# Performance work log

Hardware: AMD Instinct MI355X
Metric: run time of the kernel (lower is better)

The kernel has to match this reference:

```python
import jax, jax.numpy as jnp
import numpy as np

B, T, C = 4, 2048, 1024
H, HS = 16, 64  # n_heads, head_size; H*HS == C


def setup_inputs() -> dict:
    key = jax.random.key(0)
    ks = jax.random.split(key, 6)
    s = 0.02
    x = jax.random.normal(ks[0], (B, T, C), dtype=jnp.float32)
    Wq = jax.random.normal(ks[1], (H, C, HS), dtype=jnp.float32) * s
    Wk = jax.random.normal(ks[2], (H, C, HS), dtype=jnp.float32) * s
    Wv = jax.random.normal(ks[3], (H, C, HS), dtype=jnp.float32) * s
    Wo = jax.random.normal(ks[4], (C, C), dtype=jnp.float32) * s
    bo = jnp.zeros((C,), dtype=jnp.float32)
    return {"x": x, "Wq": Wq, "Wk": Wk, "Wv": Wv, "Wo": Wo, "bo": bo}


def reference(x, Wq, Wk, Wv, Wo, bo):
    # batched multi-head causal attention (math identical to per-head loop)
    q = jnp.einsum('btc,hcd->bhtd', x, Wq)  # [B,H,T,HS]
    k = jnp.einsum('btc,hcd->bhtd', x, Wk)
    v = jnp.einsum('btc,hcd->bhtd', x, Wv)
    scale = 1.0 / jnp.sqrt(jnp.asarray(HS, x.dtype))
    scores = jnp.einsum('bhtd,bhsd->bhts', q, k) * scale  # [B,H,T,T]
    causal = jnp.tril(jnp.ones((T, T), dtype=bool))
    scores = jnp.where(causal, scores, jnp.asarray(-jnp.inf, scores.dtype))
    attn = jax.nn.softmax(scores, axis=-1)
    out = jnp.einsum('bhts,bhsd->bhtd', attn, v)  # [B,H,T,HS]
    # concat heads along feature dim (head order == module list order)
    out = out.transpose(0, 2, 1, 3).reshape(B, T, C)
    return out @ Wo.T + bo
```

## Files before the change

### kernel.cpp

```cpp
#include <hip/hip_runtime.h>

typedef __attribute__((ext_vector_type(8))) short v8s;
typedef __attribute__((ext_vector_type(4))) short v4s;
typedef __attribute__((ext_vector_type(4))) float v4f;

static __device__ __forceinline__ short f2bf(float f) {
  union { float f; unsigned u; } c; c.f = f;
  unsigned r = c.u + 0x7fffu + ((c.u >> 16) & 1u);
  return (short)(r >> 16);
}

static __device__ __forceinline__ unsigned pk_bf16(float a, float b) {
  union { float f; unsigned u; } ca, cb; ca.f = a; cb.f = b;
  return ((ca.u + 0x8000u) >> 16) | ((cb.u + 0x8000u) & 0xffff0000u);
}

#if __has_builtin(__builtin_amdgcn_exp2f)
#define EXP2(x) __builtin_amdgcn_exp2f(x)
#else
#define EXP2(x) exp2f(x)
#endif

#define GLDS(gp, lp) __builtin_amdgcn_global_load_lds( \
    (const __attribute__((address_space(1))) void*)(gp), \
    (__attribute__((address_space(3))) void*)(lp), 16, 0, 0)


__global__ __launch_bounds__(256) void cast_f32_bf16(const float* __restrict__ src,
                                                     short* __restrict__ dst) {
  int idx = (blockIdx.x * 256 + threadIdx.x) * 4;
  float4 v = *(const float4*)(src + idx);
  v4s o; o.x = f2bf(v.x); o.y = f2bf(v.y); o.z = f2bf(v.z); o.w = f2bf(v.w);
  *(v4s*)(dst + idx) = o;
}

__global__ __launch_bounds__(256) void build_wt(const float* __restrict__ Wq,
                                                const float* __restrict__ Wk,
                                                const float* __restrict__ Wv,
                                                short* __restrict__ Wt) {
  __shared__ float tile[64][65];
  int blk = blockIdx.x;
  int sel = blk >> 8, rest = blk & 255;
  int h = rest >> 4, kt = rest & 15;
  const float* W = (sel == 0) ? Wq : ((sel == 1) ? Wk : Wv);
  int k0 = kt * 64;
  int tid = threadIdx.x;
  for (int i = 0; i < 4; ++i) {
    int c = i * 256 + tid;
    int row = c >> 4, c4 = (c & 15) * 4;
    float4 v = *(const float4*)(W + (size_t)h * 65536 + (size_t)(k0 + row) * 64 + c4);
    tile[row][c4 + 0] = v.x; tile[row][c4 + 1] = v.y;
    tile[row][c4 + 2] = v.z; tile[row][c4 + 3] = v.w;
  }
  __syncthreads();
  for (int i = 0; i < 2; ++i) {
    int c = i * 256 + tid;
    int d = c >> 3, k8 = (c & 7) * 8;
    v8s o;
    for (int j = 0; j < 8; ++j) o[j] = f2bf(tile[k8 + j][d]);
    *(v8s*)(Wt + (size_t)(sel * 1024 + h * 64 + d) * 1024 + k0 + k8) = o;
  }
}


__global__ __launch_bounds__(512) void gemm_qkv(const short* __restrict__ Xb,
                                                const short* __restrict__ Wt,
                                                short* __restrict__ Qo,
                                                short* __restrict__ Ko,
                                                short* __restrict__ Vt) {
  __shared__ short lds[49152];
  const int tid = threadIdx.x;
  const int lane = tid & 63, quad = lane >> 4, l16 = lane & 15;
  const int wave = tid >> 6;
  const int m0 = blockIdx.x * 256, n0 = blockIdx.y * 128;
  const int wm = (wave >> 1) * 64, wn = (wave & 1) * 64;

  const int r0 = tid >> 2, cbs = (tid & 3) ^ ((r0 >> 1) & 3);
  const size_t offA0 = (size_t)(m0 + r0) * 1024 + cbs * 8;
  const size_t offB0 = (size_t)(n0 + r0) * 1024 + cbs * 8;

  int aoff[4], boff[4];
#pragma unroll
  for (int mt = 0; mt < 4; ++mt) {
    int row = wm + mt * 16 + l16;
    aoff[mt] = row * 32 + (quad ^ ((row >> 1) & 3)) * 8;
  }
#pragma unroll
  for (int nt = 0; nt < 4; ++nt) {
    int row = wn + nt * 16 + l16;
    boff[nt] = row * 32 + (quad ^ ((row >> 1) & 3)) * 8;
  }

  v4f acc[4][4];
#pragma unroll
  for (int i = 0; i < 4; ++i)
#pragma unroll
    for (int j = 0; j < 4; ++j) acc[i][j] = (v4f){0.f, 0.f, 0.f, 0.f};

#pragma unroll
  for (int t = 0; t < 3; ++t) {
    GLDS(Xb + offA0 + t * 32, lds + t * 8192 + tid * 8);
    GLDS(Xb + offA0 + 131072 + t * 32, lds + t * 8192 + 4096 + tid * 8);
    GLDS(Wt + offB0 + t * 32, lds + 32768 + t * 4096 + tid * 8);
  }
  asm volatile("s_waitcnt vmcnt(6)" ::: "memory");
  __builtin_amdgcn_s_barrier();

#pragma unroll 4
  for (int t = 0; t < 32; ++t) {
    const int p = t & 3;
    int tn = t + 3; if (tn > 31) tn = 31;
    const int pn = (t + 3) & 3;
    const short* lAp = lds + p * 8192;
    const short* lBp = lds + 32768 + p * 4096;

    GLDS(Xb + offA0 + tn * 32, lds + pn * 8192 + tid * 8);
    GLDS(Xb + offA0 + 131072 + tn * 32, lds + pn * 8192 + 4096 + tid * 8);
    v8s a[4], b[2];
#pragma unroll
    for (int mt = 0; mt < 4; ++mt) a[mt] = *(const v8s*)(lAp + aoff[mt]);
    b[0] = *(const v8s*)(lBp + boff[0]);
    b[1] = *(const v8s*)(lBp + boff[1]);
    __builtin_amdgcn_s_setprio(1);
#pragma unroll
    for (int mt = 0; mt < 4; ++mt) {
      acc[mt][0] = __builtin_amdgcn_mfma_f32_16x16x32_bf16(a[mt], b[0], acc[mt][0], 0, 0, 0);
      acc[mt][1] = __builtin_amdgcn_mfma_f32_16x16x32_bf16(a[mt], b[1], acc[mt][1], 0, 0, 0);
    }
    __builtin_amdgcn_s_setprio(0);

    GLDS(Wt + offB0 + tn * 32, lds + 32768 + pn * 4096 + tid * 8);
    b[0] = *(const v8s*)(lBp + boff[2]);
    b[1] = *(const v8s*)(lBp + boff[3]);
    __builtin_amdgcn_s_setprio(1);
#pragma unroll
    for (int mt = 0; mt < 4; ++mt) {
      acc[mt][2] = __builtin_amdgcn_mfma_f32_16x16x32_bf16(a[mt], b[0], acc[mt][2], 0, 0, 0);
      acc[mt][3] = __builtin_amdgcn_mfma_f32_16x16x32_bf16(a[mt], b[1], acc[mt][3], 0, 0, 0);
    }
    __builtin_amdgcn_s_setprio(0);

    asm volatile("s_waitcnt vmcnt(6) lgkmcnt(0)" ::: "memory");
    __builtin_amdgcn_s_barrier();
  }

  const int selu = n0 >> 10;
  if (selu < 2) {
    short* obase = (selu == 0) ? Qo : Ko;
#pragma unroll
    for (int nt = 0; nt < 4; ++nt) {
      int n = (n0 + wn + nt * 16 + l16) & 1023;
      int h = n >> 6, d = n & 63;
#pragma unroll
      for (int mt = 0; mt < 4; ++mt) {
        int m = m0 + wm + mt * 16 + quad * 4;
        int b_ = m >> 11, tt = m & 2047;
        size_t base = (size_t)((b_ * 16 + h) * 2048 + tt) * 64 + d;
#pragma unroll
        for (int r = 0; r < 4; ++r)
          obase[base + (size_t)r * 64] = f2bf(acc[mt][nt][r]);
      }
    }
  } else {
#pragma unroll
    for (int nt = 0; nt < 4; ++nt) {
      int n = (n0 + wn + nt * 16 + l16) & 1023;
      int h = n >> 6, d = n & 63;
#pragma unroll
      for (int mt = 0; mt < 4; ++mt) {
        int m = m0 + wm + mt * 16 + quad * 4;
        int b_ = m >> 11, tt = m & 2047;
        int2 dw;
        dw.x = (int)pk_bf16(acc[mt][nt][0], acc[mt][nt][1]);
        dw.y = (int)pk_bf16(acc[mt][nt][2], acc[mt][nt][3]);
        *(int2*)(Vt + ((size_t)(b_ * 16 + h) * 64 + d) * 2048 + tt) = dw;
      }
    }
  }
}


__global__ __launch_bounds__(256, 2) void attn(const short* __restrict__ Q,
                                               const short* __restrict__ K,
                                               const short* __restrict__ Vt,
                                               short* __restrict__ AO) {
  __shared__ short lK[64 * 64];
  __shared__ short lV[64 * 64];
  __shared__ short lP[4 * 32 * 72];
  const int tid = threadIdx.x;
  const int w = tid >> 6, lane = tid & 63, quad = lane >> 4, l16 = lane & 15;
  const int bh = blockIdx.x & 63, pr = blockIdx.x >> 6;
  const float kexp = 0.18033688011112042f;
  const unsigned psel = 0x07060302u;
  short* pw = lP + w * (32 * 72);
  const size_t qkbase = (size_t)bh * 2048 * 64;
  const size_t vtbase = (size_t)bh * 64 * 2048;
  const int b_ = bh >> 4, h = bh & 15;

  const int r0 = tid >> 3, cp = tid & 7;
  const int cl0 = cp ^ (r0 & 7);
  const int r1 = r0 + 32;
  const int cl1 = cp ^ (r1 & 7);

  const int swz = l16 & 7;
  const int ph0 = (quad ^ swz) * 8;
  const int ph1 = ((quad + 4) ^ swz) * 8;

  for (int phase = 0; phase < 2; ++phase) {
    const int c = phase ? (15 - pr) : pr;
    const int qc = c * 128 + w * 32;

    v8s bQ[2][2];
#pragma unroll
    for (int qs = 0; qs < 2; ++qs) {
      const short* qb = Q + qkbase + (size_t)(qc + qs * 16 + l16) * 64 + quad * 8;
      bQ[qs][0] = *(const v8s*)(qb);
      bQ[qs][1] = *(const v8s*)(qb + 32);
    }
    v4f accO[2][4];
#pragma unroll
    for (int qs = 0; qs < 2; ++qs)
      for (int g = 0; g < 4; ++g) accO[qs][g] = (v4f){0.f, 0.f, 0.f, 0.f};
    float lrun[2] = {0.f, 0.f};

    const int nst = 2 * c + 2;
    for (int kt = 0; kt < nst; ++kt) {
      const int kb = kt * 64;
      __syncthreads();
      GLDS(K + qkbase + (size_t)(kb + r0) * 64 + cl0 * 8, lK + tid * 8);
      GLDS(K + qkbase + (size_t)(kb + r1) * 64 + cl1 * 8, lK + tid * 8 + 2048);
      GLDS(Vt + vtbase + (size_t)r0 * 2048 + kb + cl0 * 8, lV + tid * 8);
      GLDS(Vt + vtbase + (size_t)r1 * 2048 + kb + cl1 * 8, lV + tid * 8 + 2048);
      __syncthreads();

      const bool act0 = kb < qc + 16;
      const bool act1 = kb < qc + 32;
      if (!act1) continue;

      v8s aK[4][2];
#pragma unroll
      for (int mt = 0; mt < 4; ++mt) {
        const short* kr = lK + (mt * 16 + l16) * 64;
        aK[mt][0] = *(const v8s*)(kr + ph0);
        aK[mt][1] = *(const v8s*)(kr + ph1);
      }
#pragma unroll
      for (int qs = 0; qs < 2; ++qs) {
        if (qs == 0 ? !act0 : false) continue;
        const int rbase = qc + qs * 16;
        v4f sT[4];
#pragma unroll
        for (int mt = 0; mt < 4; ++mt) {
          v4f t = (v4f){0.f, 0.f, 0.f, 0.f};
          t = __builtin_amdgcn_mfma_f32_16x16x32_bf16(aK[mt][0], bQ[qs][0], t, 0, 0, 0);
          t = __builtin_amdgcn_mfma_f32_16x16x32_bf16(aK[mt][1], bQ[qs][1], t, 0, 0, 0);
          sT[mt] = t;
        }
        if (kb + 63 >= rbase) {
          const int kq = kb + quad * 4 - (rbase + l16);
#pragma unroll
          for (int mt = 0; mt < 4; ++mt)
#pragma unroll
            for (int r = 0; r < 4; ++r)
              if (kq + mt * 16 + r > 0) sT[mt][r] = -__builtin_inff();
        }
        float ls = lrun[qs];
#pragma unroll
        for (int mt = 0; mt < 4; ++mt) {
          float p0 = EXP2(sT[mt][0] * kexp);
          float p1 = EXP2(sT[mt][1] * kexp);
          float p2 = EXP2(sT[mt][2] * kexp);
          float p3 = EXP2(sT[mt][3] * kexp);
          ls += (p0 + p1) + (p2 + p3);
          int2 dw;
          dw.x = (int)__builtin_amdgcn_perm(__float_as_uint(p1), __float_as_uint(p0), psel);
          dw.y = (int)__builtin_amdgcn_perm(__float_as_uint(p3), __float_as_uint(p2), psel);
          *(int2*)&pw[(qs * 16 + l16) * 72 + mt * 16 + quad * 4] = dw;
        }
        lrun[qs] = ls;
      }
      v8s aV[4][2];
#pragma unroll
      for (int g = 0; g < 4; ++g) {
        const short* vr = lV + (g * 16 + l16) * 64;
        aV[g][0] = *(const v8s*)(vr + ph0);
        aV[g][1] = *(const v8s*)(vr + ph1);
      }
#pragma unroll
      for (int qs = 0; qs < 2; ++qs) {
        if (qs == 0 ? !act0 : false) continue;
        v8s bP0 = *(const v8s*)&pw[(qs * 16 + l16) * 72 + quad * 8];
        v8s bP1 = *(const v8s*)&pw[(qs * 16 + l16) * 72 + 32 + quad * 8];
#pragma unroll
        for (int g = 0; g < 4; ++g) {
          accO[qs][g] = __builtin_amdgcn_mfma_f32_16x16x32_bf16(aV[g][0], bP0, accO[qs][g], 0, 0, 0);
          accO[qs][g] = __builtin_amdgcn_mfma_f32_16x16x32_bf16(aV[g][1], bP1, accO[qs][g], 0, 0, 0);
        }
      }
    }

#pragma unroll
    for (int qs = 0; qs < 2; ++qs) {
      float ls = lrun[qs];
      ls += __shfl_xor(ls, 16);
      ls += __shfl_xor(ls, 32);
      float inv = __builtin_amdgcn_rcpf(ls);
      int t = qc + qs * 16 + l16;
      short* ao = AO + ((size_t)(b_ * 2048 + t)) * 1024 + h * 64 + quad * 4;
#pragma unroll
      for (int g = 0; g < 4; ++g) {
        int2 dw;
        dw.x = (int)pk_bf16(accO[qs][g][0] * inv, accO[qs][g][1] * inv);
        dw.y = (int)pk_bf16(accO[qs][g][2] * inv, accO[qs][g][3] * inv);
        *(int2*)(ao + g * 16) = dw;
      }
    }
  }
}


__global__ __launch_bounds__(256) void gemm_out(const short* __restrict__ AO,
                                                const short* __restrict__ Wot,
                                                const float* __restrict__ bo,
                                                float* __restrict__ out) {
  __shared__ short lA[128 * 32];
  __shared__ short lB[128 * 32];
  const int tid = threadIdx.x;
  const int lane = tid & 63, quad = lane >> 4, l16 = lane & 15;
  const int wave = tid >> 6;
  const int m0 = blockIdx.x * 128, n0 = blockIdx.y * 128;
  const int wm = (wave >> 1) * 64, wn = (wave & 1) * 64;
  v4f acc[4][4];
  for (int i = 0; i < 4; ++i)
    for (int j = 0; j < 4; ++j) acc[i][j] = (v4f){0.f, 0.f, 0.f, 0.f};

  for (int k0 = 0; k0 < 1024; k0 += 32) {
    __syncthreads();
    for (int i = 0; i < 2; ++i) {
      int c = i * 256 + tid;
      int row = c >> 2, kc = c & 3;
      GLDS(AO + (size_t)(m0 + row) * 1024 + k0 + kc * 8, lA + c * 8);
      GLDS(Wot + (size_t)(n0 + row) * 1024 + k0 + kc * 8, lB + c * 8);
    }
    __syncthreads();
    v8s a[4], b[4];
    for (int mt = 0; mt < 4; ++mt) a[mt] = *(const v8s*)&lA[(wm + mt * 16 + l16) * 32 + quad * 8];
    for (int nt = 0; nt < 4; ++nt) b[nt] = *(const v8s*)&lB[(wn + nt * 16 + l16) * 32 + quad * 8];
    for (int mt = 0; mt < 4; ++mt)
      for (int nt = 0; nt < 4; ++nt)
        acc[mt][nt] = __builtin_amdgcn_mfma_f32_16x16x32_bf16(a[mt], b[nt], acc[mt][nt], 0, 0, 0);
  }

  for (int nt = 0; nt < 4; ++nt) {
    int n = n0 + wn + nt * 16 + l16;
    float bias = bo[n];
    for (int mt = 0; mt < 4; ++mt)
      for (int r = 0; r < 4; ++r) {
        int m = m0 + wm + mt * 16 + quad * 4 + r;
        out[(size_t)m * 1024 + n] = acc[mt][nt][r] + bias;
      }
  }
}


extern "C" void kernel_launch(void* const* d_in, const int* in_sizes, int n_in,
                              void* d_out, int out_size, void* d_ws, size_t ws_size,
                              hipStream_t stream) {
  const float* x  = (const float*)d_in[0];
  const float* Wq = (const float*)d_in[1];
  const float* Wk = (const float*)d_in[2];
  const float* Wv = (const float*)d_in[3];
  const float* Wo = (const float*)d_in[4];
  const float* bo = (const float*)d_in[5];
  float* out = (float*)d_out;
  char* ws = (char*)d_ws;

  short* Xb  = (short*)(ws);
  short* Wt  = (short*)(ws + (16u << 20));
  short* Wot = (short*)(ws + (22u << 20));
  short* Q   = (short*)(ws + (24u << 20));
  short* K   = (short*)(ws + (40u << 20));
  short* Vt  = (short*)(ws + (56u << 20));

  cast_f32_bf16<<<8192, 256, 0, stream>>>(x, Xb);
  cast_f32_bf16<<<1024, 256, 0, stream>>>(Wo, Wot);
  build_wt<<<768, 256, 0, stream>>>(Wq, Wk, Wv, Wt);
  gemm_qkv<<<dim3(32, 24), 512, 0, stream>>>(Xb, Wt, Q, K, Vt);
  attn<<<dim3(512), 256, 0, stream>>>(Q, K, Vt, Xb);
  gemm_out<<<dim3(64, 8), 256, 0, stream>>>(Xb, Wot, bo, out);
}
```

Measured before the change: 243.0 us.

## Restructure QKV GEMM into 256x256 tiles with K=64 phased ping-pong pipeline

The fused QKV projection GEMM moves from 256x128 tiles with K=32 steps and a 4-stage ring to 256x256 tiles with K=64 steps. LDS is split into two ping-pong buffers, and each k-tile runs four phases that interleave half-tile global-to-LDS staging with MFMA blocks, with barriers and priority set around each phase. Each wave now holds an 8x4 accumulator block, which should roughly double arithmetic intensity per LDS load. The grid is 1D with a remap that groups tiles sharing the same activation rows. The larger register footprint and 128KB of LDS limit the kernel to one block per CU, and with 384 blocks the tail wave may be uneven.

```diff
diff --git a/kernel.cpp b/kernel.cpp
--- a/kernel.cpp
+++ b/kernel.cpp
@@ -63,121 +63,159 @@
 }
 
 
+#define STAGE_A(P, H, T)                                                          \
+  GLDS(Xb + sA0 + (H) * 131072 + (size_t)(T) * 64,                                \
+       lds + (P) * 16384 + (H) * 8192 + tid * 8);                                 \
+  GLDS(Xb + sA0 + (H) * 131072 + 65536 + (size_t)(T) * 64,                        \
+       lds + (P) * 16384 + (H) * 8192 + 4096 + tid * 8)
+
+#define STAGE_B(P, H, T)                                                          \
+  GLDS(Wt + sB0 + (H) * 131072 + (size_t)(T) * 64,                                \
+       lds + 32768 + (P) * 16384 + (H) * 8192 + tid * 8);                         \
+  GLDS(Wt + sB0 + (H) * 131072 + 65536 + (size_t)(T) * 64,                        \
+       lds + 32768 + (P) * 16384 + (H) * 8192 + 4096 + tid * 8)
+
+#define PH_MID()                                                                  \
+  __builtin_amdgcn_s_barrier();                                                   \
+  asm volatile("s_waitcnt lgkmcnt(0)" ::: "memory");                              \
+  __builtin_amdgcn_sched_barrier(0);                                              \
+  __builtin_amdgcn_s_setprio(1)
+
+#define PH_END()                                                                  \
+  __builtin_amdgcn_s_setprio(0);                                                  \
+  __builtin_amdgcn_s_barrier()
+
+#define MFMA8(AR, BC)                                                             \
+  _Pragma("unroll") for (int fa = 0; fa < 4; ++fa)                                \
+  _Pragma("unroll") for (int fb = 0; fb < 2; ++fb) {                              \
+    acc[AR + fa][BC + fb] = __builtin_amdgcn_mfma_f32_16x16x32_bf16(              \
+        a[fa][0], b[fb][0], acc[AR + fa][BC + fb], 0, 0, 0);                      \
+    acc[AR + fa][BC + fb] = __builtin_amdgcn_mfma_f32_16x16x32_bf16(              \
+        a[fa][1], b[fb][1], acc[AR + fa][BC + fb], 0, 0, 0);                      \
+  }
+
+#define LOAD_A(P, MH)                                                             \
+  _Pragma("unroll") for (int fa = 0; fa < 4; ++fa) {                              \
+    const short* ap = lds + (P) * 16384 + abase + (MH) * 4096 + fa * 1024;        \
+    a[fa][0] = *(const v8s*)(ap + csw0);                                          \
+    a[fa][1] = *(const v8s*)(ap + csw1);                                          \
+  }
+
+#define LOAD_B(P, NH)                                                             \
+  _Pragma("unroll") for (int fb = 0; fb < 2; ++fb) {                              \
+    const short* bp = lds + 32768 + (P) * 16384 + bbase + (NH) * 2048 + fb * 1024;\
+    b[fb][0] = *(const v8s*)(bp + csw0);                                          \
+    b[fb][1] = *(const v8s*)(bp + csw1);                                          \
+  }
+
+#define KTILE(P, PN, TN1, TN2)                                                    \
+                                                         \
+  LOAD_A(P, 0); LOAD_B(P, 0);                                                     \
+  STAGE_A(PN, 1, TN1);                                                            \
+  PH_MID(); MFMA8(0, 0); PH_END();                                                \
+                                                         \
+  LOAD_B(P, 1);                                                                   \
+  STAGE_B(PN, 0, TN1);                                                            \
+  PH_MID(); MFMA8(0, 2); PH_END();                                                \
+                                                         \
+  LOAD_A(P, 1);                                                                   \
+  STAGE_A(P, 0, TN2);                                                             \
+  PH_MID(); MFMA8(4, 2); PH_END();                                                \
+                                                         \
+  LOAD_B(P, 0);                                                                   \
+  STAGE_B(P, 1, TN2);                                                             \
+  PH_MID(); MFMA8(4, 0);                                                          \
+  __builtin_amdgcn_s_setprio(0);                                                  \
+  asm volatile("s_waitcnt vmcnt(4)" ::: "memory");                                \
+  __builtin_amdgcn_s_barrier()
+
 __global__ __launch_bounds__(512) void gemm_qkv(const short* __restrict__ Xb,
                                                 const short* __restrict__ Wt,
                                                 short* __restrict__ Qo,
                                                 short* __restrict__ Ko,
                                                 short* __restrict__ Vt) {
-  __shared__ short lds[49152];
+  __shared__ short lds[65536];
   const int tid = threadIdx.x;
   const int lane = tid & 63, quad = lane >> 4, l16 = lane & 15;
   const int wave = tid >> 6;
-  const int m0 = blockIdx.x * 256, n0 = blockIdx.y * 128;
-  const int wm = (wave >> 1) * 64, wn = (wave & 1) * 64;
-
-  const int r0 = tid >> 2, cbs = (tid & 3) ^ ((r0 >> 1) & 3);
-  const size_t offA0 = (size_t)(m0 + r0) * 1024 + cbs * 8;
-  const size_t offB0 = (size_t)(n0 + r0) * 1024 + cbs * 8;
-
-  int aoff[4], boff[4];
-#pragma unroll
-  for (int mt = 0; mt < 4; ++mt) {
-    int row = wm + mt * 16 + l16;
-    aoff[mt] = row * 32 + (quad ^ ((row >> 1) & 3)) * 8;
-  }
-#pragma unroll
-  for (int nt = 0; nt < 4; ++nt) {
-    int row = wn + nt * 16 + l16;
-    boff[nt] = row * 32 + (quad ^ ((row >> 1) & 3)) * 8;
-  }
-
-  v4f acc[4][4];
-#pragma unroll
-  for (int i = 0; i < 4; ++i)
+  const int bid = blockIdx.x;
+  const int wg = (bid & 7) * 48 + (bid >> 3);
+  const int m0 = (wg & 31) * 256, n0 = (wg >> 5) * 256;
+
+  const int cbl = (tid & 7) ^ ((tid >> 3) & 7);
+  const size_t sA0 = (size_t)(m0 + (tid >> 3)) * 1024 + cbl * 8;
+  const size_t sB0 = (size_t)(n0 + (tid >> 3)) * 1024 + cbl * 8;
+
+  const int abase = (wave >> 2) * 8192 + l16 * 64;
+  const int bbase = ((wave & 3) >> 1) * 8192 + ((wave & 1) * 64 + l16) * 64;
+  const int csw0 = (quad ^ (l16 & 7)) * 8;
+  const int csw1 = ((4 + quad) ^ (l16 & 7)) * 8;
+
+  v4f acc[8][4];
+#pragma unroll
+  for (int i = 0; i < 8; ++i)
 #pragma unroll
     for (int j = 0; j < 4; ++j) acc[i][j] = (v4f){0.f, 0.f, 0.f, 0.f};
-
-#pragma unroll
-  for (int t = 0; t < 3; ++t) {
-    GLDS(Xb + offA0 + t * 32, lds + t * 8192 + tid * 8);
-    GLDS(Xb + offA0 + 131072 + t * 32, lds + t * 8192 + 4096 + tid * 8);
-    GLDS(Wt + offB0 + t * 32, lds + 32768 + t * 4096 + tid * 8);
-  }
-  asm volatile("s_waitcnt vmcnt(6)" ::: "memory");
+  v8s a[4][2], b[2][2];
+
+  STAGE_A(0, 0, 0); STAGE_B(0, 0, 0); STAGE_A(0, 1, 0); STAGE_B(0, 1, 0);
+  STAGE_A(1, 0, 1); STAGE_B(1, 1, 1);
+  asm volatile("s_waitcnt vmcnt(4)" ::: "memory");
   __builtin_amdgcn_s_barrier();
 
-#pragma unroll 4
-  for (int t = 0; t < 32; ++t) {
-    const int p = t & 3;
-    int tn = t + 3; if (tn > 31) tn = 31;
-    const int pn = (t + 3) & 3;
-    const short* lAp = lds + p * 8192;
-    const short* lBp = lds + 32768 + p * 4096;
-
-    GLDS(Xb + offA0 + tn * 32, lds + pn * 8192 + tid * 8);
-    GLDS(Xb + offA0 + 131072 + tn * 32, lds + pn * 8192 + 4096 + tid * 8);
-    v8s a[4], b[2];
-#pragma unroll
-    for (int mt = 0; mt < 4; ++mt) a[mt] = *(const v8s*)(lAp + aoff[mt]);
-    b[0] = *(const v8s*)(lBp + boff[0]);
-    b[1] = *(const v8s*)(lBp + boff[1]);
-    __builtin_amdgcn_s_setprio(1);
-#pragma unroll
-    for (int mt = 0; mt < 4; ++mt) {
-      acc[mt][0] = __builtin_amdgcn_mfma_f32_16x16x32_bf16(a[mt], b[0], acc[mt][0], 0, 0, 0);
-      acc[mt][1] = __builtin_amdgcn_mfma_f32_16x16x32_bf16(a[mt], b[1], acc[mt][1], 0, 0, 0);
-    }
-    __builtin_amdgcn_s_setprio(0);
-
-    GLDS(Wt + offB0 + tn * 32, lds + 32768 + pn * 4096 + tid * 8);
-    b[0] = *(const v8s*)(lBp + boff[2]);
-    b[1] = *(const v8s*)(lBp + boff[3]);
-    __builtin_amdgcn_s_setprio(1);
-#pragma unroll
-    for (int mt = 0; mt < 4; ++mt) {
-      acc[mt][2] = __builtin_amdgcn_mfma_f32_16x16x32_bf16(a[mt], b[0], acc[mt][2], 0, 0, 0);
-      acc[mt][3] = __builtin_amdgcn_mfma_f32_16x16x32_bf16(a[mt], b[1], acc[mt][3], 0, 0, 0);
-    }
-    __builtin_amdgcn_s_setprio(0);
-
-    asm volatile("s_waitcnt vmcnt(6) lgkmcnt(0)" ::: "memory");
-    __builtin_amdgcn_s_barrier();
-  }
+#pragma unroll 1
+  for (int tt = 0; tt < 8; ++tt) {
+    const int t0 = tt * 2;
+    const int t2 = (t0 + 2 < 16) ? t0 + 2 : 15;
+    const int t3 = (t0 + 3 < 16) ? t0 + 3 : 15;
+    KTILE(0, 1, t0 + 1, t2);
+    KTILE(1, 0, t2, t3);
+  }
+  asm volatile("s_waitcnt vmcnt(0)" ::: "memory");
 
   const int selu = n0 >> 10;
   if (selu < 2) {
     short* obase = (selu == 0) ? Qo : Ko;
 #pragma unroll
-    for (int nt = 0; nt < 4; ++nt) {
-      int n = (n0 + wn + nt * 16 + l16) & 1023;
+    for (int FB = 0; FB < 4; ++FB) {
+      int n = (n0 + (wave & 3) * 64 + FB * 16 + l16) & 1023;
       int h = n >> 6, d = n & 63;
 #pragma unroll
-      for (int mt = 0; mt < 4; ++mt) {
-        int m = m0 + wm + mt * 16 + quad * 4;
-        int b_ = m >> 11, tt = m & 2047;
-        size_t base = (size_t)((b_ * 16 + h) * 2048 + tt) * 64 + d;
+      for (int FA = 0; FA < 8; ++FA) {
+        int m = m0 + (wave >> 2) * 128 + FA * 16 + quad * 4;
+        int b_ = m >> 11, tt_ = m & 2047;
+        size_t base = (size_t)((b_ * 16 + h) * 2048 + tt_) * 64 + d;
 #pragma unroll
         for (int r = 0; r < 4; ++r)
-          obase[base + (size_t)r * 64] = f2bf(acc[mt][nt][r]);
+          obase[base + (size_t)r * 64] = f2bf(acc[FA][FB][r]);
       }
     }
   } else {
 #pragma unroll
-    for (int nt = 0; nt < 4; ++nt) {
-      int n = (n0 + wn + nt * 16 + l16) & 1023;
+    for (int FB = 0; FB < 4; ++FB) {
+      int n = (n0 + (wave & 3) * 64 + FB * 16 + l16) & 1023;
       int h = n >> 6, d = n & 63;
 #pragma unroll
-      for (int mt = 0; mt < 4; ++mt) {
-        int m = m0 + wm + mt * 16 + quad * 4;
-        int b_ = m >> 11, tt = m & 2047;
+      for (int FA = 0; FA < 8; ++FA) {
+        int m = m0 + (wave >> 2) * 128 + FA * 16 + quad * 4;
+        int b_ = m >> 11, tt_ = m & 2047;
         int2 dw;
-        dw.x = (int)pk_bf16(acc[mt][nt][0], acc[mt][nt][1]);
-        dw.y = (int)pk_bf16(acc[mt][nt][2], acc[mt][nt][3]);
-        *(int2*)(Vt + ((size_t)(b_ * 16 + h) * 64 + d) * 2048 + tt) = dw;
-      }
-    }
-  }
-}
+        dw.x = (int)pk_bf16(acc[FA][FB][0], acc[FA][FB][1]);
+        dw.y = (int)pk_bf16(acc[FA][FB][2], acc[FA][FB][3]);
+        *(int2*)(Vt + ((size_t)(b_ * 16 + h) * 64 + d) * 2048 + tt_) = dw;
+      }
+    }
+  }
+}
+
+#undef KTILE
+#undef LOAD_A
+#undef LOAD_B
+#undef MFMA8
+#undef PH_MID
+#undef PH_END
+#undef STAGE_A
+#undef STAGE_B
 
 
 __global__ __launch_bounds__(256, 2) void attn(const short* __restrict__ Q,
@@ -385,7 +423,7 @@
   cast_f32_bf16<<<8192, 256, 0, stream>>>(x, Xb);
   cast_f32_bf16<<<1024, 256, 0, stream>>>(Wo, Wot);
   build_wt<<<768, 256, 0, stream>>>(Wq, Wk, Wv, Wt);
-  gemm_qkv<<<dim3(32, 24), 512, 0, stream>>>(Xb, Wt, Q, K, Vt);
+  gemm_qkv<<<384, 512, 0, stream>>>(Xb, Wt, Q, K, Vt);
   attn<<<dim3(512), 256, 0, stream>>>(Q, K, Vt, Xb);
-  gemm_out<<<dim3(64, 8), 256, 0, stream>>>(Xb, Wot, bo, out);
-}
+  gemm_out<<<Xb ? dim3(64, 8) : dim3(64, 8), 256, 0, stream>>>(Xb, Wot, bo, out);
+}
```

Result: no change. 247.1 us (+1.7%).
